# Performance work log

Hardware: AMD Instinct MI355X
Metric: run time of the kernel (lower is better)

## Reference

```python
import jax, jax.numpy as jnp
import numpy as np

B, S, H, V = 4, 2048, 768, 32000
HID = 100          # self.hidden_size
N_LABELS = 3
LN2 = 0.6931471805599453


def setup_inputs() -> dict:
    key = jax.random.key(0)
    ks = jax.random.split(key, 10)
    return {
        "input_ids": jax.random.randint(ks[0], (B, S), 0, V),
        "attention_mask": jnp.ones((B, S), jnp.float32),
        "sentiment": jax.random.normal(ks[1], (B, 3), jnp.float32),
        "hidden_states": jax.random.normal(ks[2], (B, S, H), jnp.float32),
        "lm_logits": jax.random.normal(ks[3], (B, S, V), jnp.float32),
        "W_ih": jax.random.normal(ks[4], (4 * HID, H + 1), jnp.float32) * 0.05,
        "W_hh": jax.random.normal(ks[5], (4 * HID, HID), jnp.float32) * 0.05,
        "b_ih": jax.random.normal(ks[6], (4 * HID,), jnp.float32) * 0.05,
        "b_hh": jax.random.normal(ks[7], (4 * HID,), jnp.float32) * 0.05,
        "cls_W": jax.random.normal(ks[8], (N_LABELS, HID + 3), jnp.float32) * 0.05,
        "cls_b": jax.random.normal(ks[9], (N_LABELS,), jnp.float32) * 0.05,
    }


def _lstm_last(x, W_ih, W_hh, b_ih, b_hh):
    # x: [B,S,D] -> last hidden state [B,HID]; PyTorch gate order i,f,g,o
    b, hid = x.shape[0], W_hh.shape[1]
    x_proj = jnp.einsum('bsd,gd->bsg', x, W_ih) + b_ih + b_hh  # [B,S,4H]

    def step(carry, xt):
        h, c = carry
        gates = xt + h @ W_hh.T
        i, f, g, o = jnp.split(gates, 4, axis=-1)
        c = jax.nn.sigmoid(f) * c + jax.nn.sigmoid(i) * jnp.tanh(g)
        h = jax.nn.sigmoid(o) * jnp.tanh(c)
        return (h, c), None

    h0 = jnp.zeros((b, hid), x.dtype)
    (hT, _), _ = jax.lax.scan(step, (h0, h0), jnp.swapaxes(x_proj, 0, 1))
    return hT


def reference(input_ids, attention_mask, sentiment, hidden_states, lm_logits,
              W_ih, W_hh, b_ih, b_hh, cls_W, cls_b):
    # surprisal: -log2(softmax(logits)[input_ids]) * mask, detached
    log_p = jax.nn.log_softmax(lm_logits, axis=-1)                       # [B,S,V]
    lp = jnp.take_along_axis(log_p, input_ids[..., None], axis=2)[..., 0]  # [B,S]
    surp = jax.lax.stop_gradient((-lp / LN2) * attention_mask)

    x = jnp.concatenate([hidden_states, surp[..., None]], axis=-1)  # [B,S,H+1]
    hT = _lstm_last(x, W_ih, W_hh, b_ih, b_hh)                      # [B,HID]
    # dropout is identity at inference
    feat = jnp.concatenate([hT, sentiment], axis=1)                 # [B,HID+3]
    return feat @ cls_W.T + cls_b                                   # [B,N_LABELS]
```

## Files before the change

kernel.cpp:

```cpp
#include <hip/hip_runtime.h>
#include <hip/hip_bf16.h>
#include <math.h>

#define B 4
#define S 2048
#define H 768
#define V 32000
#define HID 100
#define G4 400
#define M_TOT (B*S)
#define PD 2

typedef _Float16 half2_t __attribute__((ext_vector_type(2)));
typedef _Float16 half8_t __attribute__((ext_vector_type(8)));

__device__ __forceinline__ float fdot2_(half2_t a, half2_t b, float c) {
#if __has_builtin(__builtin_amdgcn_fdot2)
  return __builtin_amdgcn_fdot2(a, b, c, false);
#else
  return c + (float)a[0] * (float)b[0] + (float)a[1] * (float)b[1];
#endif
}

__device__ __forceinline__ float sigmoidf_(float x) {
  return 1.0f / (1.0f + __expf(-x));
}

__device__ __forceinline__ void lds_barrier_() {
  asm volatile("s_waitcnt lgkmcnt(0)" ::: "memory");
  __builtin_amdgcn_s_barrier();
  asm volatile("" ::: "memory");
}

__global__ __launch_bounds__(256) void surprisal_kernel(
    const float* __restrict__ logits, const int* __restrict__ ids,
    const float* __restrict__ mask, float* __restrict__ surp) {
  int row = blockIdx.x;
  const float* x = logits + (size_t)row * V;
  int tid = threadIdx.x;
  float m = -INFINITY, s = 0.0f;
  const float4* x4 = (const float4*)x;
  for (int i = tid; i < V / 4; i += 256) {
    float4 v = x4[i];
    float mv = fmaxf(fmaxf(v.x, v.y), fmaxf(v.z, v.w));
    if (mv > m) { s *= __expf(m - mv); m = mv; }
    s += __expf(v.x - m) + __expf(v.y - m) + __expf(v.z - m) + __expf(v.w - m);
  }
  #pragma unroll
  for (int off = 32; off > 0; off >>= 1) {
    float mo = __shfl_xor(m, off);
    float so = __shfl_xor(s, off);
    float mn = fmaxf(m, mo);
    s = s * __expf(m - mn) + so * __expf(mo - mn);
    m = mn;
  }
  __shared__ float sm[4], ss[4];
  int wid = tid >> 6, lane = tid & 63;
  if (lane == 0) { sm[wid] = m; ss[wid] = s; }
  __syncthreads();
  if (tid == 0) {
    float M = sm[0], Ssum = ss[0];
    #pragma unroll
    for (int w = 1; w < 4; ++w) {
      float mo = sm[w], so = ss[w];
      float mn = fmaxf(M, mo);
      Ssum = Ssum * __expf(M - mn) + so * __expf(mo - mn);
      M = mn;
    }
    float xid = x[ids[row]];
    surp[row] = (M + __logf(Ssum) - xid) * 1.4426950408889634f * mask[row];
  }
}

#define BM 64
#define BN 64
#define BK 32

__global__ __launch_bounds__(256) void xproj_kernel(
    const float* __restrict__ A,
    const float* __restrict__ surp,
    const float* __restrict__ W,
    const float* __restrict__ b_ih, const float* __restrict__ b_hh,
    float* __restrict__ xproj) {
  __shared__ float As[BK][BM];
  __shared__ float Bs[BK][BN];
  int tid = threadIdx.x;
  int m0 = blockIdx.x * BM;
  int n0 = blockIdx.y * BN;
  int tx = tid & 15, ty = tid >> 4;
  float acc[4][4] = {};
  for (int k0 = 0; k0 < H; k0 += BK) {
    #pragma unroll
    for (int l = 0; l < 2; ++l) {
      int idx = tid + l * 256;
      int row = idx >> 3;
      int kq = idx & 7;
      float4 v = *(const float4*)&A[(size_t)(m0 + row) * H + k0 + kq * 4];
      As[kq * 4 + 0][row] = v.x;
      As[kq * 4 + 1][row] = v.y;
      As[kq * 4 + 2][row] = v.z;
      As[kq * 4 + 3][row] = v.w;
    }
    #pragma unroll
    for (int l = 0; l < 8; ++l) {
      int idx = tid + l * 256;
      int n = idx >> 5;
      int kk = idx & 31;
      int gn = n0 + n;
      Bs[kk][n] = (gn < G4) ? W[(size_t)gn * (H + 1) + k0 + kk] : 0.0f;
    }
    __syncthreads();
    #pragma unroll
    for (int k = 0; k < BK; ++k) {
      float4 a = *(const float4*)&As[k][ty * 4];
      float4 bq = *(const float4*)&Bs[k][tx * 4];
      float av[4] = {a.x, a.y, a.z, a.w};
      float bv[4] = {bq.x, bq.y, bq.z, bq.w};
      #pragma unroll
      for (int i = 0; i < 4; ++i)
        #pragma unroll
        for (int j = 0; j < 4; ++j)
          acc[i][j] += av[i] * bv[j];
    }
    __syncthreads();
  }
  #pragma unroll
  for (int i = 0; i < 4; ++i) {
    int gm = m0 + ty * 4 + i;
    float sv = surp[gm];
    #pragma unroll
    for (int j = 0; j < 4; ++j) {
      int gn = n0 + tx * 4 + j;
      if (gn < G4) {
        float val = acc[i][j] + sv * W[(size_t)gn * (H + 1) + H] + b_ih[gn] + b_hh[gn];
        int g = gn / HID, k = gn % HID;
        int pn = 4 * k + (((g & 1) << 1) | (g >> 1));
        xproj[(size_t)gm * G4 + pn] = val;
      }
    }
  }
}

#define NH2 52
__global__ __launch_bounds__(256, 1) void lstm_kernel(
    const float* __restrict__ xproj,
    const float* __restrict__ W_hh,
    const float* __restrict__ sent,
    const float* __restrict__ cls_W,
    const float* __restrict__ cls_b,
    float* __restrict__ out) {
  int b = blockIdx.x;
  int tid = threadIdx.x;
  __shared__ __align__(16) _Float16 hb0[2 * NH2];
  __shared__ __align__(16) _Float16 hb1[2 * NH2];

  bool active = tid < 200;
  int q = active ? tid : 199;
  int k = q >> 1;
  bool odd = (q & 1) != 0;
  int rA = odd ? (HID + k) : k;
  int rB = odd ? (3 * HID + k) : (2 * HID + k);

  half2_t wA[NH2], wB[NH2];
  {
    const float* pA = W_hh + (size_t)rA * HID;
    const float* pB = W_hh + (size_t)rB * HID;
    #pragma unroll
    for (int j = 0; j < 50; ++j) {
      wA[j] = half2_t{(_Float16)pA[2 * j], (_Float16)pA[2 * j + 1]};
      wB[j] = half2_t{(_Float16)pB[2 * j], (_Float16)pB[2 * j + 1]};
    }
    #pragma unroll
    for (int j = 50; j < NH2; ++j) { wA[j] = half2_t{0, 0}; wB[j] = half2_t{0, 0}; }
  }

  float c_reg = 0.0f;
  if (tid < 2 * NH2) { hb0[tid] = (_Float16)0; hb1[tid] = (_Float16)0; }
  __syncthreads();

  const float* xp = xproj + (size_t)b * S * G4;
  float2 xr[PD];
  #pragma unroll
  for (int d = 0; d < PD; ++d)
    xr[d] = ((const float2*)(xp + (size_t)d * G4))[q];

  #pragma unroll 2
  for (int t = 0; t < S; ++t) {
    int slot = t & (PD - 1);
    const half8_t* hr = (t & 1) ? (const half8_t*)hb0 : (const half8_t*)hb1;
    _Float16* hw = (t & 1) ? hb1 : hb0;

    float2 xv = xr[slot];
    {
      int tp = (t + PD < S) ? (t + PD) : (S - 1);
      xr[slot] = ((const float2*)(xp + (size_t)tp * G4))[q];
    }

    float a0 = 0.f, a1 = 0.f, b0 = 0.f, b1 = 0.f;
    #pragma unroll
    for (int j = 0; j < 13; ++j) {
      half8_t hv = hr[j];
      half2_t h0 = {hv[0], hv[1]}, h1 = {hv[2], hv[3]};
      half2_t h2 = {hv[4], hv[5]}, h3 = {hv[6], hv[7]};
      a0 = fdot2_(wA[4 * j + 0], h0, a0);
      b0 = fdot2_(wB[4 * j + 0], h0, b0);
      a1 = fdot2_(wA[4 * j + 1], h1, a1);
      b1 = fdot2_(wB[4 * j + 1], h1, b1);
      a0 = fdot2_(wA[4 * j + 2], h2, a0);
      b0 = fdot2_(wB[4 * j + 2], h2, b0);
      a1 = fdot2_(wA[4 * j + 3], h3, a1);
      b1 = fdot2_(wB[4 * j + 3], h3, b1);
    }
    float aA = a0 + a1 + xv.x;
    float aB = b0 + b1 + xv.y;

    float vA = sigmoidf_(aA);
    float sB = sigmoidf_(odd ? aB : 2.0f * aB);
    float vB = odd ? sB : (2.0f * sB - 1.0f);

    float f_n = __shfl_xor(vA, 1);
    float o_n = __shfl_xor(vB, 1);

    c_reg = f_n * c_reg + vA * vB;
    float tc = 2.0f * sigmoidf_(2.0f * c_reg) - 1.0f;
    float h = o_n * tc;
    if (active && !odd) hw[k] = (_Float16)h;

    lds_barrier_();
  }

  if (tid < 3) {
    float acc = cls_b[tid];
    const float* cw = cls_W + tid * (HID + 3);
    #pragma unroll
    for (int j = 0; j < HID; ++j) acc += cw[j] * (float)hb1[j];
    #pragma unroll
    for (int k2 = 0; k2 < 3; ++k2) acc += cw[HID + k2] * sent[b * 3 + k2];
    out[b * 3 + tid] = acc;
  }
}

extern "C" void kernel_launch(void* const* d_in, const int* in_sizes, int n_in,
                              void* d_out, int out_size, void* d_ws, size_t ws_size,
                              hipStream_t stream) {
  const int*   input_ids = (const int*)d_in[0];
  const float* mask      = (const float*)d_in[1];
  const float* sent      = (const float*)d_in[2];
  const float* hs        = (const float*)d_in[3];
  const float* logits    = (const float*)d_in[4];
  const float* W_ih      = (const float*)d_in[5];
  const float* W_hh      = (const float*)d_in[6];
  const float* b_ih      = (const float*)d_in[7];
  const float* b_hh      = (const float*)d_in[8];
  const float* cls_W     = (const float*)d_in[9];
  const float* cls_b     = (const float*)d_in[10];
  float* out = (float*)d_out;

  float* surp  = (float*)d_ws;
  float* xproj = surp + M_TOT;

  surprisal_kernel<<<M_TOT, 256, 0, stream>>>(logits, input_ids, mask, surp);
  xproj_kernel<<<dim3(M_TOT / BM, (G4 + BN - 1) / BN), 256, 0, stream>>>(
      hs, surp, W_ih, b_ih, b_hh, xproj);
  lstm_kernel<<<B, 256, 0, stream>>>(xproj, W_hh, sent, cls_W, cls_b, out);
}
```

Before: 1.403 ms.

## Compute LSTM recurrent matvec with MFMA instead of per-thread fdot2

Replaces the per-thread fp16 dot-product loops in the LSTM recurrence with MFMA 16x16x32 instructions. W_hh stays in registers as A fragments spread across 4 waves, and h is fed as the B operand with only column 0 populated. Gate pre-activations go through an LDS buffer, so each timestep now needs two barriers instead of one. Most of each MFMA's work is wasted on zero columns, and the added barrier and LDS round trip may cancel out the lower instruction count on this latency-bound serial loop.

```diff
diff --git a/kernel.cpp b/kernel.cpp
--- a/kernel.cpp
+++ b/kernel.cpp
@@ -10,17 +10,11 @@
 #define G4 400
 #define M_TOT (B*S)
 #define PD 2
+#define NTILE 7
 
 typedef _Float16 half2_t __attribute__((ext_vector_type(2)));
 typedef _Float16 half8_t __attribute__((ext_vector_type(8)));
-
-__device__ __forceinline__ float fdot2_(half2_t a, half2_t b, float c) {
-#if __has_builtin(__builtin_amdgcn_fdot2)
-  return __builtin_amdgcn_fdot2(a, b, c, false);
-#else
-  return c + (float)a[0] * (float)b[0] + (float)a[1] * (float)b[1];
-#endif
-}
+typedef float float4_t __attribute__((ext_vector_type(4)));
 
 __device__ __forceinline__ float sigmoidf_(float x) {
   return 1.0f / (1.0f + __expf(-x));
@@ -141,7 +135,6 @@
   }
 }
 
-#define NH2 52
 __global__ __launch_bounds__(256, 1) void lstm_kernel(
     const float* __restrict__ xproj,
     const float* __restrict__ W_hh,
@@ -151,31 +144,41 @@
     float* __restrict__ out) {
   int b = blockIdx.x;
   int tid = threadIdx.x;
-  __shared__ __align__(16) _Float16 hb0[2 * NH2];
-  __shared__ __align__(16) _Float16 hb1[2 * NH2];
+  __shared__ __align__(16) _Float16 h_lds[128];
+  __shared__ __align__(16) float gates_lds[G4];
+
+  int lane = tid & 63;
+  int w = tid >> 6;
+  int col = lane & 15;
+  int kg = lane >> 4;
+
+  half8_t afrag[NTILE][4];
+  #pragma unroll
+  for (int tt = 0; tt < NTILE; ++tt) {
+    int tau = NTILE * w + tt;
+    if (tau > 24) tau = 24;
+    int row = 16 * tau + col;
+    const float* wp = W_hh + (size_t)((row & 3) * HID + (row >> 2)) * HID;
+    #pragma unroll
+    for (int kt = 0; kt < 4; ++kt) {
+      half8_t v;
+      #pragma unroll
+      for (int e = 0; e < 8; ++e) {
+        int k = kt * 32 + kg * 8 + e;
+        v[e] = (k < HID) ? (_Float16)wp[k] : (_Float16)0.f;
+      }
+      afrag[tt][kt] = v;
+    }
+  }
 
   bool active = tid < 200;
   int q = active ? tid : 199;
   int k = q >> 1;
   bool odd = (q & 1) != 0;
-  int rA = odd ? (HID + k) : k;
-  int rB = odd ? (3 * HID + k) : (2 * HID + k);
-
-  half2_t wA[NH2], wB[NH2];
-  {
-    const float* pA = W_hh + (size_t)rA * HID;
-    const float* pB = W_hh + (size_t)rB * HID;
-    #pragma unroll
-    for (int j = 0; j < 50; ++j) {
-      wA[j] = half2_t{(_Float16)pA[2 * j], (_Float16)pA[2 * j + 1]};
-      wB[j] = half2_t{(_Float16)pB[2 * j], (_Float16)pB[2 * j + 1]};
-    }
-    #pragma unroll
-    for (int j = 50; j < NH2; ++j) { wA[j] = half2_t{0, 0}; wB[j] = half2_t{0, 0}; }
-  }
+  int par = q & 1;
 
   float c_reg = 0.0f;
-  if (tid < 2 * NH2) { hb0[tid] = (_Float16)0; hb1[tid] = (_Float16)0; }
+  if (tid < 128) h_lds[tid] = (_Float16)0;
   __syncthreads();
 
   const float* xp = xproj + (size_t)b * S * G4;
@@ -187,44 +190,46 @@
   #pragma unroll 2
   for (int t = 0; t < S; ++t) {
     int slot = t & (PD - 1);
-    const half8_t* hr = (t & 1) ? (const half8_t*)hb0 : (const half8_t*)hb1;
-    _Float16* hw = (t & 1) ? hb1 : hb0;
-
     float2 xv = xr[slot];
     {
       int tp = (t + PD < S) ? (t + PD) : (S - 1);
       xr[slot] = ((const float2*)(xp + (size_t)tp * G4))[q];
     }
 
-    float a0 = 0.f, a1 = 0.f, b0 = 0.f, b1 = 0.f;
-    #pragma unroll
-    for (int j = 0; j < 13; ++j) {
-      half8_t hv = hr[j];
-      half2_t h0 = {hv[0], hv[1]}, h1 = {hv[2], hv[3]};
-      half2_t h2 = {hv[4], hv[5]}, h3 = {hv[6], hv[7]};
-      a0 = fdot2_(wA[4 * j + 0], h0, a0);
-      b0 = fdot2_(wB[4 * j + 0], h0, b0);
-      a1 = fdot2_(wA[4 * j + 1], h1, a1);
-      b1 = fdot2_(wB[4 * j + 1], h1, b1);
-      a0 = fdot2_(wA[4 * j + 2], h2, a0);
-      b0 = fdot2_(wB[4 * j + 2], h2, b0);
-      a1 = fdot2_(wA[4 * j + 3], h3, a1);
-      b1 = fdot2_(wB[4 * j + 3], h3, b1);
-    }
-    float aA = a0 + a1 + xv.x;
-    float aB = b0 + b1 + xv.y;
-
+    half8_t bfrag[4];
+    #pragma unroll
+    for (int kt = 0; kt < 4; ++kt) {
+      half8_t v = {0, 0, 0, 0, 0, 0, 0, 0};
+      if (col == 0) v = *(const half8_t*)(h_lds + kt * 32 + kg * 8);
+      bfrag[kt] = v;
+    }
+    #pragma unroll
+    for (int tt = 0; tt < NTILE; ++tt) {
+      float4_t acc = {0.f, 0.f, 0.f, 0.f};
+      #pragma unroll
+      for (int kt = 0; kt < 4; ++kt)
+        acc = __builtin_amdgcn_mfma_f32_16x16x32_f16(afrag[tt][kt], bfrag[kt],
+                                                     acc, 0, 0, 0);
+      int tau = NTILE * w + tt;
+      if (col == 0 && tau < 25)
+        *(float4_t*)(gates_lds + 16 * tau + 4 * kg) = acc;
+    }
+
+    lds_barrier_();
+
+    float gA = gates_lds[4 * k + par];
+    float gB = gates_lds[4 * k + par + 2];
+    float aA = gA + xv.x;
+    float aB = gB + xv.y;
     float vA = sigmoidf_(aA);
     float sB = sigmoidf_(odd ? aB : 2.0f * aB);
     float vB = odd ? sB : (2.0f * sB - 1.0f);
-
     float f_n = __shfl_xor(vA, 1);
     float o_n = __shfl_xor(vB, 1);
-
     c_reg = f_n * c_reg + vA * vB;
     float tc = 2.0f * sigmoidf_(2.0f * c_reg) - 1.0f;
     float h = o_n * tc;
-    if (active && !odd) hw[k] = (_Float16)h;
+    if (active && !odd) h_lds[k] = (_Float16)h;
 
     lds_barrier_();
   }
@@ -233,7 +238,7 @@
     float acc = cls_b[tid];
     const float* cw = cls_W + tid * (HID + 3);
     #pragma unroll
-    for (int j = 0; j < HID; ++j) acc += cw[j] * (float)hb1[j];
+    for (int j = 0; j < HID; ++j) acc += cw[j] * (float)h_lds[j];
     #pragma unroll
     for (int k2 = 0; k2 < 3; ++k2) acc += cw[HID + k2] * sent[b * 3 + k2];
     out[b * 3 + tid] = acc;
```

New measurement: 1.856 ms. 32.3% more time.

## Prefetch LSTM input projections in 16-step chunks staged through LDS

Applied to the files above, without the earlier changes.

The per-step global prefetch of xproj (distance 2) is replaced by a chunked scheme. Every 16 steps each thread issues 16 global loads for the next chunk into registers, writes them into a double-buffered LDS area at the chunk boundary, and each step reads its input from LDS. The aim is to hide global-memory latency on the serial recurrence's critical path. The cost is 32 extra VGPRs, about 51KB of LDS, and a burst of loads and stores every 16 steps.

```diff
diff --git a/kernel.cpp b/kernel.cpp
--- a/kernel.cpp
+++ b/kernel.cpp
@@ -9,7 +9,7 @@
 #define HID 100
 #define G4 400
 #define M_TOT (B*S)
-#define PD 2
+#define CH 16
 
 typedef _Float16 half2_t __attribute__((ext_vector_type(2)));
 typedef _Float16 half8_t __attribute__((ext_vector_type(8)));
@@ -141,7 +141,6 @@
   }
 }
 
-#define NH2 52
 __global__ __launch_bounds__(256, 1) void lstm_kernel(
     const float* __restrict__ xproj,
     const float* __restrict__ W_hh,
@@ -151,8 +150,9 @@
     float* __restrict__ out) {
   int b = blockIdx.x;
   int tid = threadIdx.x;
-  __shared__ __align__(16) _Float16 hb0[2 * NH2];
-  __shared__ __align__(16) _Float16 hb1[2 * NH2];
+  __shared__ __align__(16) _Float16 hb0[104];
+  __shared__ __align__(16) _Float16 hb1[104];
+  __shared__ __align__(16) float xs[2][CH * G4];
 
   bool active = tid < 200;
   int q = active ? tid : 199;
@@ -161,7 +161,7 @@
   int rA = odd ? (HID + k) : k;
   int rB = odd ? (3 * HID + k) : (2 * HID + k);
 
-  half2_t wA[NH2], wB[NH2];
+  half2_t wA[52], wB[52];
   {
     const float* pA = W_hh + (size_t)rA * HID;
     const float* pB = W_hh + (size_t)rB * HID;
@@ -171,35 +171,43 @@
       wB[j] = half2_t{(_Float16)pB[2 * j], (_Float16)pB[2 * j + 1]};
     }
     #pragma unroll
-    for (int j = 50; j < NH2; ++j) { wA[j] = half2_t{0, 0}; wB[j] = half2_t{0, 0}; }
+    for (int j = 50; j < 52; ++j) { wA[j] = half2_t{0, 0}; wB[j] = half2_t{0, 0}; }
   }
 
   float c_reg = 0.0f;
-  if (tid < 2 * NH2) { hb0[tid] = (_Float16)0; hb1[tid] = (_Float16)0; }
+  if (tid < 104) { hb0[tid] = (_Float16)0; hb1[tid] = (_Float16)0; }
+
+  const float* xp = xproj + (size_t)b * S * G4;
+  float2 xreg[CH];
+
+  #pragma unroll
+  for (int j = 0; j < CH; ++j)
+    xreg[j] = ((const float2*)(xp + (size_t)j * G4))[q];
+  #pragma unroll
+  for (int j = 0; j < CH; ++j)
+    *(float2*)&xs[0][j * G4 + 2 * q] = xreg[j];
   __syncthreads();
-
-  const float* xp = xproj + (size_t)b * S * G4;
-  float2 xr[PD];
-  #pragma unroll
-  for (int d = 0; d < PD; ++d)
-    xr[d] = ((const float2*)(xp + (size_t)d * G4))[q];
 
   #pragma unroll 2
   for (int t = 0; t < S; ++t) {
-    int slot = t & (PD - 1);
-    const half8_t* hr = (t & 1) ? (const half8_t*)hb0 : (const half8_t*)hb1;
+    const _Float16* hr = (t & 1) ? hb0 : hb1;
     _Float16* hw = (t & 1) ? hb1 : hb0;
 
-    float2 xv = xr[slot];
-    {
-      int tp = (t + PD < S) ? (t + PD) : (S - 1);
-      xr[slot] = ((const float2*)(xp + (size_t)tp * G4))[q];
-    }
+    if ((t & (CH - 1)) == 0) {
+      int tn = t + CH;
+      #pragma unroll
+      for (int j = 0; j < CH; ++j) {
+        int tl = tn + j; if (tl > S - 1) tl = S - 1;
+        xreg[j] = ((const float2*)(xp + (size_t)tl * G4))[q];
+      }
+    }
+
+    float2 xv = *(const float2*)&xs[(t >> 4) & 1][(t & (CH - 1)) * G4 + 2 * q];
 
     float a0 = 0.f, a1 = 0.f, b0 = 0.f, b1 = 0.f;
     #pragma unroll
     for (int j = 0; j < 13; ++j) {
-      half8_t hv = hr[j];
+      half8_t hv = *(const half8_t*)(hr + 8 * j);
       half2_t h0 = {hv[0], hv[1]}, h1 = {hv[2], hv[3]};
       half2_t h2 = {hv[4], hv[5]}, h3 = {hv[6], hv[7]};
       a0 = fdot2_(wA[4 * j + 0], h0, a0);
@@ -225,6 +233,13 @@
     float tc = 2.0f * sigmoidf_(2.0f * c_reg) - 1.0f;
     float h = o_n * tc;
     if (active && !odd) hw[k] = (_Float16)h;
+
+    if ((t & (CH - 1)) == (CH - 1)) {
+      float* xd = xs[((t >> 4) + 1) & 1];
+      #pragma unroll
+      for (int j = 0; j < CH; ++j)
+        *(float2*)&xd[j * G4 + 2 * q] = xreg[j];
+    }
 
     lds_barrier_();
   }
```

Measured after the change: 1.552 ms. 10.6% more time.

## Run surprisal and input-projection GEMM concurrently in one launch, add rank-1 fixup

Applied to the files above, without the earlier changes.

Removes the dependency of the input projection on the surprisal column by dropping it from the GEMM epilogue. The GEMM tiles and the per-row log-softmax reductions then run as different block ranges of a single kernel, so the two can overlap. A small extra kernel adds surp*W_ih[:,H] into xproj afterwards. The cost is an extra read-modify-write pass over xproj and one more launch.

```diff
diff --git a/kernel.cpp b/kernel.cpp
--- a/kernel.cpp
+++ b/kernel.cpp
@@ -32,113 +32,129 @@
   asm volatile("" ::: "memory");
 }
 
-__global__ __launch_bounds__(256) void surprisal_kernel(
-    const float* __restrict__ logits, const int* __restrict__ ids,
-    const float* __restrict__ mask, float* __restrict__ surp) {
-  int row = blockIdx.x;
-  const float* x = logits + (size_t)row * V;
-  int tid = threadIdx.x;
-  float m = -INFINITY, s = 0.0f;
-  const float4* x4 = (const float4*)x;
-  for (int i = tid; i < V / 4; i += 256) {
-    float4 v = x4[i];
-    float mv = fmaxf(fmaxf(v.x, v.y), fmaxf(v.z, v.w));
-    if (mv > m) { s *= __expf(m - mv); m = mv; }
-    s += __expf(v.x - m) + __expf(v.y - m) + __expf(v.z - m) + __expf(v.w - m);
-  }
-  #pragma unroll
-  for (int off = 32; off > 0; off >>= 1) {
-    float mo = __shfl_xor(m, off);
-    float so = __shfl_xor(s, off);
-    float mn = fmaxf(m, mo);
-    s = s * __expf(m - mn) + so * __expf(mo - mn);
-    m = mn;
-  }
-  __shared__ float sm[4], ss[4];
-  int wid = tid >> 6, lane = tid & 63;
-  if (lane == 0) { sm[wid] = m; ss[wid] = s; }
-  __syncthreads();
-  if (tid == 0) {
-    float M = sm[0], Ssum = ss[0];
-    #pragma unroll
-    for (int w = 1; w < 4; ++w) {
-      float mo = sm[w], so = ss[w];
-      float mn = fmaxf(M, mo);
-      Ssum = Ssum * __expf(M - mn) + so * __expf(mo - mn);
-      M = mn;
-    }
-    float xid = x[ids[row]];
-    surp[row] = (M + __logf(Ssum) - xid) * 1.4426950408889634f * mask[row];
-  }
-}
-
 #define BM 64
 #define BN 64
 #define BK 32
-
-__global__ __launch_bounds__(256) void xproj_kernel(
+#define NTM (M_TOT / BM)
+#define NTN ((G4 + BN - 1) / BN)
+#define NGEMM (NTM * NTN)
+
+__global__ __launch_bounds__(256) void fused_pre_kernel(
+    const float* __restrict__ logits, const int* __restrict__ ids,
+    const float* __restrict__ mask, float* __restrict__ surp,
     const float* __restrict__ A,
-    const float* __restrict__ surp,
     const float* __restrict__ W,
     const float* __restrict__ b_ih, const float* __restrict__ b_hh,
     float* __restrict__ xproj) {
-  __shared__ float As[BK][BM];
-  __shared__ float Bs[BK][BN];
+  __shared__ float smem[BK * BM + BK * BN];
   int tid = threadIdx.x;
-  int m0 = blockIdx.x * BM;
-  int n0 = blockIdx.y * BN;
-  int tx = tid & 15, ty = tid >> 4;
-  float acc[4][4] = {};
-  for (int k0 = 0; k0 < H; k0 += BK) {
-    #pragma unroll
-    for (int l = 0; l < 2; ++l) {
-      int idx = tid + l * 256;
-      int row = idx >> 3;
-      int kq = idx & 7;
-      float4 v = *(const float4*)&A[(size_t)(m0 + row) * H + k0 + kq * 4];
-      As[kq * 4 + 0][row] = v.x;
-      As[kq * 4 + 1][row] = v.y;
-      As[kq * 4 + 2][row] = v.z;
-      As[kq * 4 + 3][row] = v.w;
-    }
-    #pragma unroll
-    for (int l = 0; l < 8; ++l) {
-      int idx = tid + l * 256;
-      int n = idx >> 5;
-      int kk = idx & 31;
-      int gn = n0 + n;
-      Bs[kk][n] = (gn < G4) ? W[(size_t)gn * (H + 1) + k0 + kk] : 0.0f;
-    }
+
+  if (blockIdx.x < NGEMM) {
+    float (*As)[BM] = (float(*)[BM])smem;
+    float (*Bs)[BN] = (float(*)[BN])(smem + BK * BM);
+    int bid = blockIdx.x;
+    int m0 = (bid / NTN) * BM;
+    int n0 = (bid % NTN) * BN;
+    int tx = tid & 15, ty = tid >> 4;
+    float acc[4][4] = {};
+    for (int k0 = 0; k0 < H; k0 += BK) {
+      #pragma unroll
+      for (int l = 0; l < 2; ++l) {
+        int idx = tid + l * 256;
+        int row = idx >> 3;
+        int kq = idx & 7;
+        float4 v = *(const float4*)&A[(size_t)(m0 + row) * H + k0 + kq * 4];
+        As[kq * 4 + 0][row] = v.x;
+        As[kq * 4 + 1][row] = v.y;
+        As[kq * 4 + 2][row] = v.z;
+        As[kq * 4 + 3][row] = v.w;
+      }
+      #pragma unroll
+      for (int l = 0; l < 8; ++l) {
+        int idx = tid + l * 256;
+        int n = idx >> 5;
+        int kk = idx & 31;
+        int gn = n0 + n;
+        Bs[kk][n] = (gn < G4) ? W[(size_t)gn * (H + 1) + k0 + kk] : 0.0f;
+      }
+      __syncthreads();
+      #pragma unroll
+      for (int k = 0; k < BK; ++k) {
+        float4 a = *(const float4*)&As[k][ty * 4];
+        float4 bq = *(const float4*)&Bs[k][tx * 4];
+        float av[4] = {a.x, a.y, a.z, a.w};
+        float bv[4] = {bq.x, bq.y, bq.z, bq.w};
+        #pragma unroll
+        for (int i = 0; i < 4; ++i)
+          #pragma unroll
+          for (int j = 0; j < 4; ++j)
+            acc[i][j] += av[i] * bv[j];
+      }
+      __syncthreads();
+    }
+    #pragma unroll
+    for (int i = 0; i < 4; ++i) {
+      int gm = m0 + ty * 4 + i;
+      #pragma unroll
+      for (int j = 0; j < 4; ++j) {
+        int gn = n0 + tx * 4 + j;
+        if (gn < G4) {
+          float val = acc[i][j] + b_ih[gn] + b_hh[gn];
+          int g = gn / HID, k = gn % HID;
+          int pn = 4 * k + (((g & 1) << 1) | (g >> 1));
+          xproj[(size_t)gm * G4 + pn] = val;
+        }
+      }
+    }
+  } else {
+    int row = blockIdx.x - NGEMM;
+    const float* x = logits + (size_t)row * V;
+    float m = -INFINITY, s = 0.0f;
+    const float4* x4 = (const float4*)x;
+    for (int i = tid; i < V / 4; i += 256) {
+      float4 v = x4[i];
+      float mv = fmaxf(fmaxf(v.x, v.y), fmaxf(v.z, v.w));
+      if (mv > m) { s *= __expf(m - mv); m = mv; }
+      s += __expf(v.x - m) + __expf(v.y - m) + __expf(v.z - m) + __expf(v.w - m);
+    }
+    #pragma unroll
+    for (int off = 32; off > 0; off >>= 1) {
+      float mo = __shfl_xor(m, off);
+      float so = __shfl_xor(s, off);
+      float mn = fmaxf(m, mo);
+      s = s * __expf(m - mn) + so * __expf(mo - mn);
+      m = mn;
+    }
+    __shared__ float sm[4], ss[4];
+    int wid = tid >> 6, lane = tid & 63;
+    if (lane == 0) { sm[wid] = m; ss[wid] = s; }
     __syncthreads();
-    #pragma unroll
-    for (int k = 0; k < BK; ++k) {
-      float4 a = *(const float4*)&As[k][ty * 4];
-      float4 bq = *(const float4*)&Bs[k][tx * 4];
-      float av[4] = {a.x, a.y, a.z, a.w};
-      float bv[4] = {bq.x, bq.y, bq.z, bq.w};
-      #pragma unroll
-      for (int i = 0; i < 4; ++i)
-        #pragma unroll
-        for (int j = 0; j < 4; ++j)
-          acc[i][j] += av[i] * bv[j];
-    }
-    __syncthreads();
-  }
-  #pragma unroll
-  for (int i = 0; i < 4; ++i) {
-    int gm = m0 + ty * 4 + i;
-    float sv = surp[gm];
-    #pragma unroll
-    for (int j = 0; j < 4; ++j) {
-      int gn = n0 + tx * 4 + j;
-      if (gn < G4) {
-        float val = acc[i][j] + sv * W[(size_t)gn * (H + 1) + H] + b_ih[gn] + b_hh[gn];
-        int g = gn / HID, k = gn % HID;
-        int pn = 4 * k + (((g & 1) << 1) | (g >> 1));
-        xproj[(size_t)gm * G4 + pn] = val;
-      }
-    }
-  }
+    if (tid == 0) {
+      float M = sm[0], Ssum = ss[0];
+      #pragma unroll
+      for (int w = 1; w < 4; ++w) {
+        float mo = sm[w], so = ss[w];
+        float mn = fmaxf(M, mo);
+        Ssum = Ssum * __expf(M - mn) + so * __expf(mo - mn);
+        M = mn;
+      }
+      float xid = x[ids[row]];
+      surp[row] = (M + __logf(Ssum) - xid) * 1.4426950408889634f * mask[row];
+    }
+  }
+}
+
+__global__ __launch_bounds__(448) void rank1_kernel(
+    const float* __restrict__ surp, const float* __restrict__ W,
+    float* __restrict__ xproj) {
+  int m = blockIdx.x;
+  int pn = threadIdx.x;
+  if (pn >= G4) return;
+  int k = pn >> 2, slot = pn & 3;
+  int g = ((slot & 1) << 1) | (slot >> 1);
+  int gn = g * HID + k;
+  float wl = W[(size_t)gn * (H + 1) + H];
+  xproj[(size_t)m * G4 + pn] += surp[m] * wl;
 }
 
 #define NH2 52
@@ -259,8 +275,8 @@
   float* surp  = (float*)d_ws;
   float* xproj = surp + M_TOT;
 
-  surprisal_kernel<<<M_TOT, 256, 0, stream>>>(logits, input_ids, mask, surp);
-  xproj_kernel<<<dim3(M_TOT / BM, (G4 + BN - 1) / BN), 256, 0, stream>>>(
-      hs, surp, W_ih, b_ih, b_hh, xproj);
+  fused_pre_kernel<<<NGEMM + M_TOT, 256, 0, stream>>>(
+      logits, input_ids, mask, surp, hs, W_ih, b_ih, b_hh, xproj);
+  rank1_kernel<<<M_TOT, 448, 0, stream>>>(surp, W_ih, xproj);
   lstm_kernel<<<B, 256, 0, stream>>>(xproj, W_hh, sent, cls_W, cls_b, out);
 }
```

After: 1.419 ms. Within noise of the previous version (+1.2%).
